# Kernel tuning notes

Measured on AMD Instinct MI355X. Metric: run time of the kernel, lower is better.

Reference implementation:

```python
import jax, jax.numpy as jnp
import numpy as np

B, T, D = 4, 2048, 1024
H = 16
DK = D // H
SCALE = 1.0 / np.sqrt(DK)
EPS_LN = 1e-5
EPS_NORM = 1e-8


def setup_inputs() -> dict:
    key = jax.random.key(0)
    ks = jax.random.split(key, 12)
    gain = 1.0 / np.sqrt(2.0)
    # xavier_uniform bound for square [D, D] weight with gain
    bound = gain * np.sqrt(6.0 / (D + D))

    def w(k):
        return jax.random.uniform(k, (D, D), jnp.float32, -bound, bound)

    return {
        "x": jax.random.normal(ks[0], (B, T, D), jnp.float32),
        "mask": jax.random.bernoulli(ks[1], 0.1, (B, T)),  # True = masked out
        "wq": w(ks[2]), "bq": jnp.zeros((D,), jnp.float32),
        "wk": w(ks[3]), "bk": jnp.zeros((D,), jnp.float32),
        "wv": w(ks[4]), "bv": jnp.zeros((D,), jnp.float32),
        "wo": w(ks[5]), "bo": jnp.zeros((D,), jnp.float32),
        "ln_g": jnp.ones((D,), jnp.float32),
        "ln_b": jnp.zeros((D,), jnp.float32),
    }


def _layernorm(x, g, b):
    mu = jnp.mean(x, axis=-1, keepdims=True)
    var = jnp.var(x, axis=-1, keepdims=True)
    return (x - mu) * jax.lax.rsqrt(var + EPS_LN) * g + b


def _l2norm(x):
    # torch F.normalize: x / clamp_min(||x||_2, eps)
    n = jnp.sqrt(jnp.sum(x * x, axis=-1, keepdims=True))
    return x / jnp.maximum(n, EPS_NORM)


def reference(x, mask, wq, bq, wk, bk, wv, bv, wo, bo, ln_g, ln_b):
    xn = _layernorm(x, ln_g, ln_b)  # q_norm applied to shared input

    def proj(w, bias):
        y = jnp.einsum("btd,ed->bte", xn, w) + bias
        return y.reshape(B, T, H, DK).transpose(0, 2, 1, 3)  # [B,H,T,DK]

    Q = _l2norm(proj(wq, bq))
    K = _l2norm(proj(wk, bk))
    V = proj(wv, bv)

    scores = jnp.einsum("bhqd,bhkd->bhqk", Q, K) * SCALE
    scores = jnp.clip(scores, -10.0, 10.0)
    scores = jnp.where(mask[:, None, None, :], -10000.0, scores)
    scores = scores - jnp.max(scores, axis=-1, keepdims=True)
    attn = jax.nn.softmax(scores, axis=-1)

    out = jnp.einsum("bhqk,bhkd->bhqd", attn, V)
    out = out.transpose(0, 2, 1, 3).reshape(B, T, D)
    out = jnp.einsum("btd,ed->bte", out, wo) + bo
    return out * 0.5
```

## Files before the change

kernel.cpp:

```cpp
#include <hip/hip_runtime.h>
#include <hip/hip_bf16.h>
#include <cstdint>
#include <cstddef>
#include <cstring>

typedef unsigned short u16;
typedef unsigned char u8;
typedef __attribute__((ext_vector_type(8))) short short8;
typedef __attribute__((ext_vector_type(4))) float f32x4;

#define B_    4
#define T_    2048
#define D_    1024
#define H_    16
#define DK_   64
#define QSCALE_ 0.18033688011112042f

__device__ __forceinline__ float bf2f(u16 u) {
    unsigned int x = ((unsigned int)u) << 16;
    float f; __builtin_memcpy(&f, &x, 4); return f;
}
__device__ __forceinline__ u16 f2bf(float f) {
    unsigned int x; __builtin_memcpy(&x, &f, 4);
    x += 0x7fffu + ((x >> 16) & 1u);
    return (u16)(x >> 16);
}
__device__ __forceinline__ unsigned pack_bf16_hu(float lo, float hi) {
    unsigned a, b;
    __builtin_memcpy(&a, &lo, 4);
    __builtin_memcpy(&b, &hi, 4);
    return __builtin_amdgcn_perm(b + 0x8000u, a + 0x8000u, 0x07060302u);
}

__device__ __forceinline__ int sniff_flag(const u16* __restrict__ x, int tid) {
    __shared__ int sc[4];
    int cnt = 0;
    for (int i = tid; i < 512; i += 256) {
        int e = (x[8 * i] >> 7) & 0xFF;
        if (e > 137 || (e >= 1 && e < 97)) cnt++;
    }
    for (int o = 1; o < 64; o <<= 1) cnt += __shfl_xor(cnt, o);
    if ((tid & 63) == 0) sc[tid >> 6] = cnt;
    __syncthreads();
    return (sc[0] + sc[1] + sc[2] + sc[3] > 128) ? 1 : 0;
}

__global__ __launch_bounds__(256) void mega_prep(
    const u16* __restrict__ x, const u8* __restrict__ m,
    const void* wq, const void* wk, const void* wv, const void* wo,
    const void* bq, const void* bk, const void* bv, const void* bo,
    const void* lng, const void* lnb,
    u16* __restrict__ wqc, u16* __restrict__ wkc,
    u16* __restrict__ wvc, u16* __restrict__ woc,
    u16* __restrict__ vecs, float* __restrict__ msk, int* flag,
    u16* __restrict__ xn)
{
    int tid = threadIdx.x;
    int f = sniff_flag(x, tid);
    int id = blockIdx.x;

    if (id < 4096) {
        int mat = id >> 10;
        const void* s = (mat == 0) ? wq : (mat == 1) ? wk : (mat == 2) ? wv : wo;
        u16* d = (mat == 0) ? wqc : (mat == 1) ? wkc : (mat == 2) ? wvc : woc;
        int i4 = (id & 1023) * 256 + tid;
        if (f) {
            float4 v = ((const float4*)s)[i4];
            ushort4 o; o.x = f2bf(v.x); o.y = f2bf(v.y); o.z = f2bf(v.z); o.w = f2bf(v.w);
            ((ushort4*)d)[i4] = o;
        } else {
            ((ushort4*)d)[i4] = ((const ushort4*)s)[i4];
        }
    } else if (id < 12288) {
        __shared__ float rs[4], rq[4];
        int row = id - 4096;
        int t = tid;
        float v[4];
        if (f) {
            float4 f4 = ((const float4*)x)[(size_t)row * 256 + t];
            v[0] = f4.x; v[1] = f4.y; v[2] = f4.z; v[3] = f4.w;
        } else {
            ushort4 uv = ((const ushort4*)x)[(size_t)row * 256 + t];
            v[0] = bf2f(uv.x); v[1] = bf2f(uv.y); v[2] = bf2f(uv.z); v[3] = bf2f(uv.w);
        }
        float s = v[0] + v[1] + v[2] + v[3];
        float q = v[0]*v[0] + v[1]*v[1] + v[2]*v[2] + v[3]*v[3];
        for (int o = 1; o < 64; o <<= 1) { s += __shfl_xor(s, o); q += __shfl_xor(q, o); }
        int wv_ = t >> 6, ln = t & 63;
        if (ln == 0) { rs[wv_] = s; rq[wv_] = q; }
        __syncthreads();
        s = rs[0] + rs[1] + rs[2] + rs[3];
        q = rq[0] + rq[1] + rq[2] + rq[3];
        float mu   = s * (1.0f / D_);
        float var  = q * (1.0f / D_) - mu * mu;
        float rstd = rsqrtf(var + 1e-5f);
        u16 o4[4];
        for (int i = 0; i < 4; i++) {
            float gv, bv_;
            if (f) { gv = ((const float*)lng)[t*4 + i]; bv_ = ((const float*)lnb)[t*4 + i]; }
            else   { gv = bf2f(((const u16*)lng)[t*4 + i]); bv_ = bf2f(((const u16*)lnb)[t*4 + i]); }
            o4[i] = f2bf((v[i] - mu) * rstd * gv + bv_);
        }
        ushort4 ov; ov.x = o4[0]; ov.y = o4[1]; ov.z = o4[2]; ov.w = o4[3];
        *(ushort4*)(xn + (size_t)row * D_ + t * 4) = ov;
    } else {
        __shared__ int sb[4];
        int k = id - 12288;
        int bits = 0;
        for (int i = tid; i < B_ * T_; i += 256)
            if (m[i]) bits |= (i & 7);
        for (int o = 1; o < 64; o <<= 1) bits |= __shfl_xor(bits, o);
        if ((tid & 63) == 0) sb[tid >> 6] = bits;
        __syncthreads();
        bits = sb[0] | sb[1] | sb[2] | sb[3];
        int stride = (bits & 1) ? 1 : (bits & 2) ? 2 : (bits & 4) ? 4 : 8;
        for (int i = tid; i < 1024; i += 256) {
            int idx = k * 1024 + i;
            msk[idx] = m[(size_t)idx * stride] ? -200.f : 0.f;
        }
        if (k == 0) {
            if (tid == 0) *flag = f;
            const void* ss[6] = {bq, bk, bv, bo, lng, lnb};
            for (int t = 0; t < 6; t++) {
                const void* s = ss[t];
                for (int i = tid; i < 1024; i += 256)
                    vecs[t * 1024 + i] = f ? f2bf(((const float*)s)[i]) : ((const u16*)s)[i];
            }
        }
    }
}

__global__ __launch_bounds__(256) void gemm_bt(
    const u16* __restrict__ A,
    const u16* __restrict__ W0, const u16* __restrict__ W1, const u16* __restrict__ W2,
    const u16* __restrict__ bias_all, int bias_idx0,
    u16* __restrict__ C0, u16* __restrict__ C1, u16* __restrict__ C2,
    float scale, const int* __restrict__ flag, int use_flag, int qkv_mode)
{
    const int K = 1024, N = 1024;
    const u16* W; const u16* bias; u16* C;
    if (blockIdx.z == 0)      { W = W0; bias = bias_all + (size_t)bias_idx0 * 1024;       C = C0; }
    else if (blockIdx.z == 1) { W = W1; bias = bias_all + (size_t)(bias_idx0 + 1) * 1024; C = C1; }
    else                      { W = W2; bias = bias_all + (size_t)(bias_idx0 + 2) * 1024; C = C2; }

    __shared__ u16 As[128 * 32];
    __shared__ u16 Bs[128 * 32];

    int tid  = threadIdx.x;
    int wave = tid >> 6, lane = tid & 63;
    int wm = wave >> 1, wn = wave & 1;
    int quad = lane >> 4, l16 = lane & 15;
    int bm = blockIdx.x * 128, bn = blockIdx.y * 128;

    f32x4 acc[4][4];
    const f32x4 fz = {0.f, 0.f, 0.f, 0.f};
    for (int i = 0; i < 4; i++) for (int j = 0; j < 4; j++) acc[i][j] = fz;

    int srow = lane >> 2;
    int scol = (lane & 3) * 8;
    const u16* gA0 = A + (size_t)(bm + wave * 32 + srow) * K + scol;
    const u16* gB0 = W + (size_t)(bn + wave * 32 + srow) * K + scol;

    for (int k0 = 0; k0 < K; k0 += 32) {
        for (int i = 0; i < 2; i++) {
            __builtin_amdgcn_global_load_lds(
                (const __attribute__((address_space(1))) void*)(gA0 + (size_t)i * 16 * K + k0),
                (__attribute__((address_space(3))) void*)(As + (wave * 32 + i * 16) * 32),
                16, 0, 0);
            __builtin_amdgcn_global_load_lds(
                (const __attribute__((address_space(1))) void*)(gB0 + (size_t)i * 16 * K + k0),
                (__attribute__((address_space(3))) void*)(Bs + (wave * 32 + i * 16) * 32),
                16, 0, 0);
        }
        __syncthreads();
        short8 a[4], b[4];
        for (int i = 0; i < 4; i++)
            a[i] = *(const short8*)(As + (wm * 64 + i * 16 + l16) * 32 + quad * 8);
        for (int j = 0; j < 4; j++)
            b[j] = *(const short8*)(Bs + (wn * 64 + j * 16 + l16) * 32 + quad * 8);
        for (int i = 0; i < 4; i++)
            for (int j = 0; j < 4; j++)
                acc[i][j] = __builtin_amdgcn_mfma_f32_16x16x32_bf16(a[i], b[j], acc[i][j], 0, 0, 0);
        __syncthreads();
    }

    if (qkv_mode) {
        if (blockIdx.z == 2) {
            for (int j = 0; j < 4; j++) {
                int col = bn + wn * 64 + j * 16 + l16;
                int h = col >> 6, d = col & 63;
                float bi = bf2f(bias[col]);
                for (int i = 0; i < 4; i++) {
                    int row0 = bm + wm * 64 + i * 16 + quad * 4;
                    int bq = row0 >> 11, t0 = row0 & 2047;
                    ushort4 pk;
                    pk.x = f2bf(acc[i][j][0] + bi); pk.y = f2bf(acc[i][j][1] + bi);
                    pk.z = f2bf(acc[i][j][2] + bi); pk.w = f2bf(acc[i][j][3] + bi);
                    *(ushort4*)(C + ((size_t)((bq * 16 + h) * 64 + d)) * 2048 + t0) = pk;
                }
            }
        } else {
            float sc2 = (blockIdx.z == 0) ? QSCALE_ : 1.0f;
            float bi[4];
            for (int j = 0; j < 4; j++) bi[j] = bf2f(bias[bn + wn * 64 + j * 16 + l16]);
            for (int i = 0; i < 4; i++) {
                int row0 = bm + wm * 64 + i * 16 + quad * 4;
                for (int r = 0; r < 4; r++) {
                    float v[4]; float s = 0.f;
                    for (int j = 0; j < 4; j++) { v[j] = acc[i][j][r] + bi[j]; s += v[j] * v[j]; }
                    s += __shfl_xor(s, 1); s += __shfl_xor(s, 2);
                    s += __shfl_xor(s, 4); s += __shfl_xor(s, 8);
                    float scl = sc2 / fmaxf(sqrtf(s), 1e-8f);
                    for (int j = 0; j < 4; j++) {
                        int col = bn + wn * 64 + j * 16 + l16;
                        C[(size_t)(row0 + r) * N + col] = f2bf(v[j] * scl);
                    }
                }
            }
        }
        return;
    }

    int f32out = use_flag ? *flag : 0;
    for (int j = 0; j < 4; j++) {
        int col = bn + wn * 64 + j * 16 + l16;
        float bi = bf2f(bias[col]);
        for (int i = 0; i < 4; i++) {
            int row0 = bm + wm * 64 + i * 16 + quad * 4;
            for (int r = 0; r < 4; r++) {
                float o = (acc[i][j][r] + bi) * scale;
                if (f32out) ((float*)C)[(size_t)(row0 + r) * N + col] = o;
                else        C[(size_t)(row0 + r) * N + col] = f2bf(o);
            }
        }
    }
}

__global__ __launch_bounds__(256, 4) void attn_kernel(
    const u16* __restrict__ Q, const u16* __restrict__ Kg,
    const u16* __restrict__ Vt, const float* __restrict__ msk,
    u16* __restrict__ Oout)
{
    __shared__ __align__(16) u16 Ks[2 * 64 * 64];
    __shared__ __align__(16) u16 VTs[2 * 64 * 64];

    int tid  = threadIdx.x;
    int wave = tid >> 6, lane = tid & 63;
    int quad = lane >> 4, l16 = lane & 15;
    int q0 = blockIdx.y * 128;
    int b  = blockIdx.x >> 4, h = blockIdx.x & 15;
    const size_t base  = (size_t)b * T_ * D_ + h * DK_;
    const size_t vbase = (size_t)((b * 16 + h) * 64) * T_;

    short8 qa[2][2];
    for (int g = 0; g < 2; g++) {
        const u16* qrow = Q + base + (size_t)(q0 + wave * 32 + g * 16 + l16) * D_;
        qa[g][0] = *(const short8*)(qrow + quad * 8);
        qa[g][1] = *(const short8*)(qrow + 32 + quad * 8);
    }

    int sr  = tid >> 3;
    int sc8 = tid & 7;
    const float* mq = msk + b * T_ + quad * 8;

    int r0 = sr, r1 = sr + 32;
    int rho0 = (r0 & 32) + ((r0 >> 2) & 1) * 16 + ((r0 >> 3) & 3) * 4 + (r0 & 3);
    int rho1 = (r1 & 32) + ((r1 >> 2) & 1) * 16 + ((r1 >> 3) & 3) * 4 + (r1 & 3);
    u16* ksw0 = Ks  + rho0 * 64 + ((sc8 ^ (rho0 & 7)) * 8);
    u16* ksw1 = Ks  + rho1 * 64 + ((sc8 ^ (rho1 & 7)) * 8);
    u16* vsw0 = VTs + r0 * 64 + ((sc8 ^ (r0 & 7)) * 8);
    u16* vsw1 = VTs + r1 * 64 + ((sc8 ^ (r1 & 7)) * 8);
    const u16* kg0 = Kg + base + (size_t)r0 * D_ + sc8 * 8;
    const u16* kg1 = Kg + base + (size_t)r1 * D_ + sc8 * 8;
    const u16* vg0 = Vt + vbase + (size_t)r0 * T_ + sc8 * 8;
    const u16* vg1 = Vt + vbase + (size_t)r1 * T_ + sc8 * 8;

    *(short8*)ksw0 = *(const short8*)kg0;
    *(short8*)ksw1 = *(const short8*)kg1;
    *(short8*)vsw0 = *(const short8*)vg0;
    *(short8*)vsw1 = *(const short8*)vg1;
    __syncthreads();

    const u16* kr_lo = Ks + l16 * 64 + ((quad ^ (l16 & 7)) * 8);
    const u16* kr_hi = Ks + l16 * 64 + (((4 + quad) ^ (l16 & 7)) * 8);
    const u16* vr0 = VTs + l16 * 64 + ((quad ^ (l16 & 7)) * 8);
    const u16* vr1 = VTs + l16 * 64 + (((4 + quad) ^ (l16 & 7)) * 8);

    f32x4 o_acc[2][4];
    const f32x4 fz = {0.f, 0.f, 0.f, 0.f};
    for (int g = 0; g < 2; g++) for (int j = 0; j < 4; j++) o_acc[g][j] = fz;
    float rowsum[2] = {0.f, 0.f};

#define TILE_BODY(CUR, NXT, KT) do {                                            \
    int ktn = ((KT) + 64) & (T_ - 1);                                           \
    short8 kpre0 = *(const short8*)(kg0 + (size_t)ktn * D_);                    \
    short8 kpre1 = *(const short8*)(kg1 + (size_t)ktn * D_);                    \
    short8 vpre0 = *(const short8*)(vg0 + ktn);                                 \
    short8 vpre1 = *(const short8*)(vg1 + ktn);                                 \
    f32x4 pmt[2][2];                                                            \
    for (int j2 = 0; j2 < 2; j2++)                                              \
        for (int s = 0; s < 2; s++)                                             \
            pmt[j2][s] = *(const f32x4*)(mq + (KT) + j2 * 32 + s * 4);          \
    for (int j2 = 0; j2 < 2; j2++) {                                            \
        unsigned pw[2][4];                                                      \
        for (int s = 0; s < 2; s++) {                                           \
            short8 kb0 = *(const short8*)(kr_lo + (CUR) * 4096 + (j2 * 32 + s * 16) * 64); \
            short8 kb1 = *(const short8*)(kr_hi + (CUR) * 4096 + (j2 * 32 + s * 16) * 64); \
            for (int g = 0; g < 2; g++) {                                       \
                f32x4 s4 = __builtin_amdgcn_mfma_f32_16x16x32_bf16(kb0, qa[g][0], pmt[j2][s], 0, 0, 0); \
                s4       = __builtin_amdgcn_mfma_f32_16x16x32_bf16(kb1, qa[g][1], s4, 0, 0, 0); \
                float p0 = __builtin_exp2f(s4[0]);                              \
                float p1 = __builtin_exp2f(s4[1]);                              \
                float p2 = __builtin_exp2f(s4[2]);                              \
                float p3 = __builtin_exp2f(s4[3]);                              \
                rowsum[g] += (p0 + p1) + (p2 + p3);                             \
                pw[g][s * 2]     = pack_bf16_hu(p0, p1);                        \
                pw[g][s * 2 + 1] = pack_bf16_hu(p2, p3);                        \
            }                                                                   \
        }                                                                       \
        short8 pb[2];                                                           \
        __builtin_memcpy(&pb[0], &pw[0][0], 16);                                \
        __builtin_memcpy(&pb[1], &pw[1][0], 16);                                \
        const u16* vr = (j2 ? vr1 : vr0) + (CUR) * 4096;                        \
        for (int jd = 0; jd < 4; jd++) {                                        \
            short8 vv = *(const short8*)(vr + jd * 16 * 64);                    \
            o_acc[0][jd] = __builtin_amdgcn_mfma_f32_16x16x32_bf16(vv, pb[0], o_acc[0][jd], 0, 0, 0); \
            o_acc[1][jd] = __builtin_amdgcn_mfma_f32_16x16x32_bf16(vv, pb[1], o_acc[1][jd], 0, 0, 0); \
        }                                                                       \
    }                                                                           \
    *(short8*)(ksw0 + (NXT) * 4096) = kpre0;                                    \
    *(short8*)(ksw1 + (NXT) * 4096) = kpre1;                                    \
    *(short8*)(vsw0 + (NXT) * 4096) = vpre0;                                    \
    *(short8*)(vsw1 + (NXT) * 4096) = vpre1;                                    \
    __syncthreads();                                                            \
} while (0)

    for (int kt = 0; kt < T_; kt += 128) {
        TILE_BODY(0, 1, kt);
        TILE_BODY(1, 0, kt + 64);
    }
#undef TILE_BODY

    for (int g = 0; g < 2; g++) {
        float l = rowsum[g];
        l += __shfl_xor(l, 16);
        l += __shfl_xor(l, 32);
        float inv = 1.0f / fmaxf(l, 1e-20f);
        size_t orow = base + (size_t)(q0 + wave * 32 + g * 16 + l16) * D_;
        for (int jd = 0; jd < 4; jd++) {
            ushort4 pk;
            pk.x = f2bf(o_acc[g][jd][0] * inv);
            pk.y = f2bf(o_acc[g][jd][1] * inv);
            pk.z = f2bf(o_acc[g][jd][2] * inv);
            pk.w = f2bf(o_acc[g][jd][3] * inv);
            *(ushort4*)(Oout + orow + jd * 16 + quad * 4) = pk;
        }
    }
}

extern "C" void kernel_launch(void* const* d_in, const int* in_sizes, int n_in,
                              void* d_out, int out_size, void* d_ws, size_t ws_size,
                              hipStream_t stream)
{
    const void* x    = d_in[0];
    const u8*   mask = (const u8*)d_in[1];
    const void* wq   = d_in[2];
    const void* bq   = d_in[3];
    const void* wk   = d_in[4];
    const void* bk   = d_in[5];
    const void* wv   = d_in[6];
    const void* bv   = d_in[7];
    const void* wo   = d_in[8];
    const void* bo   = d_in[9];
    const void* lng  = d_in[10];
    const void* lnb  = d_in[11];

    const size_t NTOK = (size_t)B_ * T_;
    u16* xn  = (u16*)d_ws;
    u16* Kb  = xn + NTOK * D_;
    u16* Vtb = Kb + NTOK * D_;
    u16* wqc = Vtb + NTOK * D_;
    u16* wkc = wqc + (size_t)D_ * D_;
    u16* wvc = wkc + (size_t)D_ * D_;
    u16* woc = wvc + (size_t)D_ * D_;
    u16* vecs = woc + (size_t)D_ * D_;
    float* msk = (float*)(vecs + 6 * 1024);
    int* flag = (int*)(msk + 8192);
    u16* Qb  = (u16*)d_out;

    mega_prep<<<dim3(12296), 256, 0, stream>>>(
        (const u16*)x, mask, wq, wk, wv, wo, bq, bk, bv, bo, lng, lnb,
        wqc, wkc, wvc, woc, vecs, msk, flag, xn);
    gemm_bt<<<dim3(64, 8, 3), 256, 0, stream>>>(xn, wqc, wkc, wvc, vecs, 0, Qb, Kb, Vtb, 1.0f, flag, 0, 1);
    attn_kernel<<<dim3(64, 16), 256, 0, stream>>>(Qb, Kb, Vtb, msk, xn);
    gemm_bt<<<dim3(64, 8, 1), 256, 0, stream>>>(xn, woc, woc, woc, vecs, 3, (u16*)d_out, (u16*)d_out, (u16*)d_out, 0.5f, flag, 1, 0);
}
```

Before: 359.0 us.

## Stage K/V tiles via direct global-to-LDS loads and raise MFMA wave priority

Replaces the register-staged K and V prefetch (global load into registers, later write to swizzled LDS) with global_load_lds transfers that write straight into LDS. The swizzle and row permutation now move to the global-address side, so each wave writes contiguous LDS rows. This frees registers and drops the LDS store instructions. It also wraps the MFMA/exp section in s_setprio. The risk is that the async LDS writes depend on __syncthreads and vmcnt waits for correct ordering, and the remapped addressing must reproduce the old layout exactly.

New measurement: 344.7 us. -4.0%, faster.

```diff
diff --git a/kernel.cpp b/kernel.cpp
--- a/kernel.cpp
+++ b/kernel.cpp
@@ -259,26 +259,38 @@
         qa[g][1] = *(const short8*)(qrow + 32 + quad * 8);
     }
 
-    int sr  = tid >> 3;
-    int sc8 = tid & 7;
     const float* mq = msk + b * T_ + quad * 8;
 
-    int r0 = sr, r1 = sr + 32;
-    int rho0 = (r0 & 32) + ((r0 >> 2) & 1) * 16 + ((r0 >> 3) & 3) * 4 + (r0 & 3);
-    int rho1 = (r1 & 32) + ((r1 >> 2) & 1) * 16 + ((r1 >> 3) & 3) * 4 + (r1 & 3);
-    u16* ksw0 = Ks  + rho0 * 64 + ((sc8 ^ (rho0 & 7)) * 8);
-    u16* ksw1 = Ks  + rho1 * 64 + ((sc8 ^ (rho1 & 7)) * 8);
-    u16* vsw0 = VTs + r0 * 64 + ((sc8 ^ (r0 & 7)) * 8);
-    u16* vsw1 = VTs + r1 * 64 + ((sc8 ^ (r1 & 7)) * 8);
-    const u16* kg0 = Kg + base + (size_t)r0 * D_ + sc8 * 8;
-    const u16* kg1 = Kg + base + (size_t)r1 * D_ + sc8 * 8;
-    const u16* vg0 = Vt + vbase + (size_t)r0 * T_ + sc8 * 8;
-    const u16* vg1 = Vt + vbase + (size_t)r1 * T_ + sc8 * 8;
-
-    *(short8*)ksw0 = *(const short8*)kg0;
-    *(short8*)ksw1 = *(const short8*)kg1;
-    *(short8*)vsw0 = *(const short8*)vg0;
-    *(short8*)vsw1 = *(const short8*)vg1;
+    int rL0 = wave * 8 + (lane >> 3);
+    int rL1 = rL0 + 32;
+    int c   = lane & 7;
+    int k0i = (rL0 & 32) + ((rL0 >> 2) & 3) * 8 + ((rL0 >> 4) & 1) * 4 + (rL0 & 3);
+    int k1i = (rL1 & 32) + ((rL1 >> 2) & 3) * 8 + ((rL1 >> 4) & 1) * 4 + (rL1 & 3);
+    const u16* kgs0 = Kg + base + (size_t)k0i * D_ + (c ^ (rL0 & 7)) * 8;
+    const u16* kgs1 = Kg + base + (size_t)k1i * D_ + (c ^ (rL1 & 7)) * 8;
+    const u16* vgs0 = Vt + vbase + (size_t)rL0 * T_ + (c ^ (rL0 & 7)) * 8;
+    const u16* vgs1 = Vt + vbase + (size_t)rL1 * T_ + (c ^ (rL1 & 7)) * 8;
+    u16* kd0 = Ks  + (wave * 8) * 64;
+    u16* kd1 = Ks  + (wave * 8 + 32) * 64;
+    u16* vd0 = VTs + (wave * 8) * 64;
+    u16* vd1 = VTs + (wave * 8 + 32) * 64;
+
+#define STAGE(BUF, KOFF) do {                                                   \
+    __builtin_amdgcn_global_load_lds(                                           \
+        (const __attribute__((address_space(1))) void*)(kgs0 + (size_t)(KOFF) * D_), \
+        (__attribute__((address_space(3))) void*)(kd0 + (BUF) * 4096), 16, 0, 0); \
+    __builtin_amdgcn_global_load_lds(                                           \
+        (const __attribute__((address_space(1))) void*)(kgs1 + (size_t)(KOFF) * D_), \
+        (__attribute__((address_space(3))) void*)(kd1 + (BUF) * 4096), 16, 0, 0); \
+    __builtin_amdgcn_global_load_lds(                                           \
+        (const __attribute__((address_space(1))) void*)(vgs0 + (KOFF)),         \
+        (__attribute__((address_space(3))) void*)(vd0 + (BUF) * 4096), 16, 0, 0); \
+    __builtin_amdgcn_global_load_lds(                                           \
+        (const __attribute__((address_space(1))) void*)(vgs1 + (KOFF)),         \
+        (__attribute__((address_space(3))) void*)(vd1 + (BUF) * 4096), 16, 0, 0); \
+} while (0)
+
+    STAGE(0, 0);
     __syncthreads();
 
     const u16* kr_lo = Ks + l16 * 64 + ((quad ^ (l16 & 7)) * 8);
@@ -287,20 +299,17 @@
     const u16* vr1 = VTs + l16 * 64 + (((4 + quad) ^ (l16 & 7)) * 8);
 
     f32x4 o_acc[2][4];
-    const f32x4 fz = {0.f, 0.f, 0.f, 0.f};
-    for (int g = 0; g < 2; g++) for (int j = 0; j < 4; j++) o_acc[g][j] = fz;
+    for (int g = 0; g < 2; g++) for (int j = 0; j < 4; j++) o_acc[g][j] = f32x4{0.f, 0.f, 0.f, 0.f};
     float rowsum[2] = {0.f, 0.f};
 
 #define TILE_BODY(CUR, NXT, KT) do {                                            \
     int ktn = ((KT) + 64) & (T_ - 1);                                           \
-    short8 kpre0 = *(const short8*)(kg0 + (size_t)ktn * D_);                    \
-    short8 kpre1 = *(const short8*)(kg1 + (size_t)ktn * D_);                    \
-    short8 vpre0 = *(const short8*)(vg0 + ktn);                                 \
-    short8 vpre1 = *(const short8*)(vg1 + ktn);                                 \
+    STAGE(NXT, ktn);                                                            \
     f32x4 pmt[2][2];                                                            \
     for (int j2 = 0; j2 < 2; j2++)                                              \
         for (int s = 0; s < 2; s++)                                             \
             pmt[j2][s] = *(const f32x4*)(mq + (KT) + j2 * 32 + s * 4);          \
+    __builtin_amdgcn_s_setprio(1);                                              \
     for (int j2 = 0; j2 < 2; j2++) {                                            \
         unsigned pw[2][4];                                                      \
         for (int s = 0; s < 2; s++) {                                           \
@@ -328,10 +337,7 @@
             o_acc[1][jd] = __builtin_amdgcn_mfma_f32_16x16x32_bf16(vv, pb[1], o_acc[1][jd], 0, 0, 0); \
         }                                                                       \
     }                                                                           \
-    *(short8*)(ksw0 + (NXT) * 4096) = kpre0;                                    \
-    *(short8*)(ksw1 + (NXT) * 4096) = kpre1;                                    \
-    *(short8*)(vsw0 + (NXT) * 4096) = vpre0;                                    \
-    *(short8*)(vsw1 + (NXT) * 4096) = vpre1;                                    \
+    __builtin_amdgcn_s_setprio(0);                                              \
     __syncthreads();                                                            \
 } while (0)
 
@@ -340,6 +346,7 @@
         TILE_BODY(1, 0, kt + 64);
     }
 #undef TILE_BODY
+#undef STAGE
 
     for (int g = 0; g < 2; g++) {
         float l = rowsum[g];
```
